# Kernel optimization log

Hardware: AMD Instinct MI355X
Metric: run time of the kernel (lower is better)

Reference implementation:

```python
import jax, jax.numpy as jnp
import numpy as np

B, T, IN_DIM, HID, OUT_DIM = 1024, 512, 64, 128, 1


def setup_inputs() -> dict:
    key = jax.random.key(0)
    ks = jax.random.split(key, 9)
    s_in = 1.0 / np.sqrt(IN_DIM)
    s_h = 1.0 / np.sqrt(HID)
    x = jax.random.normal(ks[0], (B, T, IN_DIM), dtype=jnp.float32)
    # layer 0 LSTM cell (eqx.nn.LSTMCell: weight_ih (4H,in), weight_hh (4H,H), bias (4H,))
    Wih0 = jax.random.uniform(ks[1], (4 * HID, IN_DIM), minval=-s_in, maxval=s_in, dtype=jnp.float32)
    Whh0 = jax.random.uniform(ks[2], (4 * HID, HID), minval=-s_h, maxval=s_h, dtype=jnp.float32)
    b0 = jax.random.uniform(ks[3], (4 * HID,), minval=-s_h, maxval=s_h, dtype=jnp.float32)
    # layer 1 LSTM cell
    Wih1 = jax.random.uniform(ks[4], (4 * HID, HID), minval=-s_h, maxval=s_h, dtype=jnp.float32)
    Whh1 = jax.random.uniform(ks[5], (4 * HID, HID), minval=-s_h, maxval=s_h, dtype=jnp.float32)
    b1 = jax.random.uniform(ks[6], (4 * HID,), minval=-s_h, maxval=s_h, dtype=jnp.float32)
    # output projection (eqx.nn.Linear: weight (out,in), bias (out,))
    Wout = jax.random.uniform(ks[7], (OUT_DIM, HID), minval=-s_h, maxval=s_h, dtype=jnp.float32)
    bout = jax.random.uniform(ks[8], (OUT_DIM,), minval=-s_h, maxval=s_h, dtype=jnp.float32)
    return {"x": x, "Wih0": Wih0, "Whh0": Whh0, "b0": b0,
            "Wih1": Wih1, "Whh1": Whh1, "b1": b1, "Wout": Wout, "bout": bout}


def _lstm_step(inp, h, c, Wih, Whh, b):
    # gates in i, f, g, o order (torch / equinox convention)
    z = inp @ Wih.T + h @ Whh.T + b  # (B, 4H)
    i, f, g, o = jnp.split(z, 4, axis=-1)
    c_new = jax.nn.sigmoid(f) * c + jax.nn.sigmoid(i) * jnp.tanh(g)
    h_new = jax.nn.sigmoid(o) * jnp.tanh(c_new)
    return h_new, c_new


def reference(x, Wih0, Whh0, b0, Wih1, Whh1, b1, Wout, bout):
    Bn = x.shape[0]
    xt = jnp.swapaxes(x, 0, 1)  # (T, B, in_dim): scan over time
    zeros = jnp.zeros((Bn, HID), dtype=x.dtype)
    init = (zeros, zeros, zeros, zeros)  # h0, c0, h1, c1

    def step(carry, x_t):
        h0, c0, h1, c1 = carry
        h0, c0 = _lstm_step(x_t, h0, c0, Wih0, Whh0, b0)
        h1, c1 = _lstm_step(h0, h1, c1, Wih1, Whh1, b1)
        return (h0, c0, h1, c1), None

    (h0, c0, h1, c1), _ = jax.lax.scan(step, init, xt)
    return h1 @ Wout.T + bout  # (B, out_dim)
```

## Files before the change

### kernel.cpp

```cpp
#include <hip/hip_runtime.h>
#include <math.h>

namespace {

constexpr int T_STEPS = 512;

typedef _Float16 h8v __attribute__((ext_vector_type(8)));
typedef _Float16 h2v __attribute__((ext_vector_type(2)));
typedef float    f4v __attribute__((ext_vector_type(4)));

__device__ __forceinline__ float sigf(float v) {
  return __builtin_amdgcn_rcpf(1.0f + __builtin_amdgcn_exp2f(-1.442695041f * v));
}
__device__ __forceinline__ float tanh_(float v) {
  return 2.0f * __builtin_amdgcn_rcpf(1.0f + __builtin_amdgcn_exp2f(-2.885390082f * v)) - 1.0f;
}

__global__ void pack_w(const float* __restrict__ Wih0, const float* __restrict__ Whh0,
                       const float* __restrict__ Wih1, const float* __restrict__ Whh1,
                       _Float16* __restrict__ PA, _Float16* __restrict__ PB) {
  int idx = blockIdx.x * 256 + threadIdx.x;
  if (idx < 98304) {
    int j = idx & 7, l = (idx >> 3) & 63;
    int f = idx >> 9;
    int ks = f % 6, wq = f / 6;
    int q = wq & 3, w = wq >> 2;
    int gate = 16 * (8 * q + w) + (l & 15);
    int k = 32 * ks + ((l >> 4) << 3) + j;
    float v = (k < 64) ? Wih0[gate * 64 + k] : Whh0[gate * 128 + (k - 64)];
    PA[idx] = (_Float16)v;
  } else if (idx < 98304 + 131072) {
    int i = idx - 98304;
    int j = i & 7, l = (i >> 3) & 63;
    int f = i >> 9;
    int ks = f & 7, wq = f >> 3;
    int q = wq & 3, w = wq >> 2;
    int gate = 16 * (8 * q + w) + (l & 15);
    int k = 32 * ks + ((l >> 4) << 3) + j;
    float v = (k < 128) ? Wih1[gate * 128 + k] : Whh1[gate * 128 + (k - 128)];
    PB[i] = (_Float16)v;
  }
}

__global__ __attribute__((amdgpu_waves_per_eu(2, 2))) __launch_bounds__(512)
void lstm_block(
    const float* __restrict__ x,
    const _Float16* __restrict__ PA, const _Float16* __restrict__ PB,
    const float* __restrict__ b0, const float* __restrict__ b1,
    const float* __restrict__ Wout, const float* __restrict__ bout,
    float* __restrict__ out) {
  extern __shared__ char smem[];
  h8v* whh = (h8v*)smem;
  _Float16(*h0t)[4][64][8] = (_Float16(*)[4][64][8])(smem + 131072);
  _Float16(*h1t)[4][64][8] = (_Float16(*)[4][64][8])(smem + 131072 + 8192);
  _Float16(*xt)[2][64][8]  = (_Float16(*)[2][64][8])(smem + 131072 + 16384);

  const int tid = threadIdx.x;
  const int g = blockIdx.x;
  const int w = tid >> 6, l = tid & 63;
  const int lo = l & 15, hi = l >> 4;
  const int unit = 16 * w + lo;
  const int kb_w = w >> 1;
  const int sub_w = (2 * w + (lo >> 3)) & 3;
  const int lanep = sub_w * 16 + hi * 4;
  const int jw = lo & 7;

  const h8v* PAv = (const h8v*)PA;
  const h8v* PBv = (const h8v*)PB;
  h8v W0[4][6], W1[4][4];
#pragma unroll
  for (int q = 0; q < 4; ++q) {
#pragma unroll
    for (int ks = 0; ks < 6; ++ks) W0[q][ks] = PAv[((w * 4 + q) * 6 + ks) * 64 + l];
#pragma unroll
    for (int ks = 0; ks < 4; ++ks) W1[q][ks] = PBv[((w * 4 + q) * 8 + ks) * 64 + l];
  }
#pragma unroll
  for (int q = 0; q < 4; ++q) {
#pragma unroll
    for (int ks = 0; ks < 6; ++ks) asm volatile("" : "+v"(W0[q][ks]));
#pragma unroll
    for (int ks = 0; ks < 4; ++ks) asm volatile("" : "+v"(W1[q][ks]));
  }
  float bA[4], bB[4];
#pragma unroll
  for (int q = 0; q < 4; ++q) { bA[q] = b0[unit + 128 * q]; bB[q] = b1[unit + 128 * q]; }
  float c0[4] = {0.f, 0.f, 0.f, 0.f}, c1[4] = {0.f, 0.f, 0.f, 0.f};

  for (int i = tid; i < 8192; i += 512) {
    int l2 = i & 63, f = i >> 6;
    int ks4 = f & 3, wq = f >> 2;
    whh[i] = PBv[(wq * 8 + 4 + ks4) * 64 + l2];
  }
  {
    unsigned int* z0 = (unsigned int*)h0t;
    unsigned int* z1 = (unsigned int*)h1t;
    for (int i = tid; i < 2048; i += 512) { z0[i] = 0u; z1[i] = 0u; }
    int row = tid >> 5, kk = (tid & 31) << 1;
    const float* xp = x + (((long)(g * 16 + row)) * T_STEPS + 0) * 64 + kk;
    float2 v = *(const float2*)xp;
    h2v pxv; pxv.x = (_Float16)v.x; pxv.y = (_Float16)v.y;
    *(h2v*)&xt[0][kk >> 5][(((kk >> 3) & 3) * 16) + row][kk & 7] = pxv;
  }
  __syncthreads();

  for (int j = 0; j <= T_STEPS; ++j) {
    const int p = j & 1;

    h8v h00 = *(const h8v*)&h0t[p][0][l][0];
    h8v h01 = *(const h8v*)&h0t[p][1][l][0];
    h8v h02 = *(const h8v*)&h0t[p][2][l][0];
    h8v h03 = *(const h8v*)&h0t[p][3][l][0];

    if (j < T_STEPS) {
      h8v ax0 = *(const h8v*)&xt[p][0][l][0];
      h8v ax1 = *(const h8v*)&xt[p][1][l][0];
      f4v accA[4];
#pragma unroll
      for (int q = 0; q < 4; ++q) {
        f4v z = {bA[q], bA[q], bA[q], bA[q]};
        z = __builtin_amdgcn_mfma_f32_16x16x32_f16(ax0, W0[q][0], z, 0, 0, 0);
        z = __builtin_amdgcn_mfma_f32_16x16x32_f16(ax1, W0[q][1], z, 0, 0, 0);
        z = __builtin_amdgcn_mfma_f32_16x16x32_f16(h00, W0[q][2], z, 0, 0, 0);
        z = __builtin_amdgcn_mfma_f32_16x16x32_f16(h01, W0[q][3], z, 0, 0, 0);
        z = __builtin_amdgcn_mfma_f32_16x16x32_f16(h02, W0[q][4], z, 0, 0, 0);
        z = __builtin_amdgcn_mfma_f32_16x16x32_f16(h03, W0[q][5], z, 0, 0, 0);
        accA[q] = z;
      }
#pragma unroll
      for (int r = 0; r < 4; ++r) {
        float cn = sigf(accA[1][r]) * c0[r] + sigf(accA[0][r]) * tanh_(accA[2][r]);
        c0[r] = cn;
        float hv = sigf(accA[3][r]) * tanh_(cn);
        h0t[p ^ 1][kb_w][lanep + r][jw] = (_Float16)hv;
      }
      if (j + 1 < T_STEPS) {
        int row = tid >> 5, kk = (tid & 31) << 1;
        const float* xp = x + (((long)(g * 16 + row)) * T_STEPS + (j + 1)) * 64 + kk;
        float2 v = *(const float2*)xp;
        h2v pxv; pxv.x = (_Float16)v.x; pxv.y = (_Float16)v.y;
        *(h2v*)&xt[p ^ 1][kk >> 5][(((kk >> 3) & 3) * 16) + row][kk & 7] = pxv;
      }
    }

    if (j >= 1) {
      h8v f10 = *(const h8v*)&h1t[p][0][l][0];
      h8v f11 = *(const h8v*)&h1t[p][1][l][0];
      h8v f12 = *(const h8v*)&h1t[p][2][l][0];
      h8v f13 = *(const h8v*)&h1t[p][3][l][0];
      f4v accB[4];
#pragma unroll
      for (int q = 0; q < 4; ++q) {
        const h8v* wb = &whh[((w * 4 + q) * 4) * 64 + l];
        h8v wh0 = wb[0];
        h8v wh1 = wb[64];
        h8v wh2 = wb[128];
        h8v wh3 = wb[192];
        f4v z = {bB[q], bB[q], bB[q], bB[q]};
        z = __builtin_amdgcn_mfma_f32_16x16x32_f16(h00, W1[q][0], z, 0, 0, 0);
        z = __builtin_amdgcn_mfma_f32_16x16x32_f16(h01, W1[q][1], z, 0, 0, 0);
        z = __builtin_amdgcn_mfma_f32_16x16x32_f16(h02, W1[q][2], z, 0, 0, 0);
        z = __builtin_amdgcn_mfma_f32_16x16x32_f16(h03, W1[q][3], z, 0, 0, 0);
        z = __builtin_amdgcn_mfma_f32_16x16x32_f16(f10, wh0, z, 0, 0, 0);
        z = __builtin_amdgcn_mfma_f32_16x16x32_f16(f11, wh1, z, 0, 0, 0);
        z = __builtin_amdgcn_mfma_f32_16x16x32_f16(f12, wh2, z, 0, 0, 0);
        z = __builtin_amdgcn_mfma_f32_16x16x32_f16(f13, wh3, z, 0, 0, 0);
        accB[q] = z;
      }
#pragma unroll
      for (int r = 0; r < 4; ++r) {
        float cn = sigf(accB[1][r]) * c1[r] + sigf(accB[0][r]) * tanh_(accB[2][r]);
        c1[r] = cn;
        float hv = sigf(accB[3][r]) * tanh_(cn);
        h1t[p ^ 1][kb_w][lanep + r][jw] = (_Float16)hv;
      }
    }
    __syncthreads();
  }

  if (tid < 16) {
    float acc = bout[0];
#pragma unroll 4
    for (int u = 0; u < 128; ++u) {
      float hval = (float)h1t[1][u >> 5][(((u >> 3) & 3) * 16) + tid][u & 7];
      acc = fmaf(hval, Wout[u], acc);
    }
    out[g * 16 + tid] = acc;
  }
}

}

extern "C" void kernel_launch(void* const* d_in, const int* in_sizes, int n_in,
                              void* d_out, int out_size, void* d_ws, size_t ws_size,
                              hipStream_t stream) {
  const float* x    = (const float*)d_in[0];
  const float* Wih0 = (const float*)d_in[1];
  const float* Whh0 = (const float*)d_in[2];
  const float* b0   = (const float*)d_in[3];
  const float* Wih1 = (const float*)d_in[4];
  const float* Whh1 = (const float*)d_in[5];
  const float* b1   = (const float*)d_in[6];
  const float* Wout = (const float*)d_in[7];
  const float* bout = (const float*)d_in[8];
  float* out = (float*)d_out;

  char* ws = (char*)d_ws;
  _Float16* PA = (_Float16*)ws;
  _Float16* PB = (_Float16*)(ws + 196608);

  const int lds_bytes = 131072 + 8192 + 8192 + 4096;
  hipFuncSetAttribute((const void*)lstm_block,
                      hipFuncAttributeMaxDynamicSharedMemorySize, lds_bytes);

  pack_w<<<dim3(896), dim3(256), 0, stream>>>(Wih0, Whh0, Wih1, Whh1, PA, PB);
  lstm_block<<<dim3(64), dim3(512), lds_bytes, stream>>>(
      x, PA, PB, b0, b1, Wout, bout, out);
}
```

Measured before the change: 1.291 ms.

## Split layer-0 and layer-1 LSTM work across separate wave groups

Doubles the block to 1024 threads so waves 0-7 compute layer 0 and waves 8-15 compute layer 1 at the same time, instead of each wave doing both layers in sequence. The input-to-hidden weights are no longer pinned in registers; each step reloads them from global memory (expected to hit in cache), which lowers register pressure enough for four waves per EU. The aim is to cut the serial dependent chain per timestep, at the cost of per-step global weight reloads and a larger barrier across more waves.

```diff
diff --git a/kernel.cpp b/kernel.cpp
--- a/kernel.cpp
+++ b/kernel.cpp
@@ -42,7 +42,7 @@
   }
 }
 
-__global__ __attribute__((amdgpu_waves_per_eu(2, 2))) __launch_bounds__(512)
+__global__ __attribute__((amdgpu_waves_per_eu(4, 4))) __launch_bounds__(1024)
 void lstm_block(
     const float* __restrict__ x,
     const _Float16* __restrict__ PA, const _Float16* __restrict__ PB,
@@ -57,8 +57,10 @@
 
   const int tid = threadIdx.x;
   const int g = blockIdx.x;
-  const int w = tid >> 6, l = tid & 63;
+  const int wv = tid >> 6, l = tid & 63;
   const int lo = l & 15, hi = l >> 4;
+  const bool isL0 = (wv < 8);
+  const int w = isL0 ? wv : (wv - 8);
   const int unit = 16 * w + lo;
   const int kb_w = w >> 1;
   const int sub_w = (2 * w + (lo >> 3)) & 3;
@@ -67,27 +69,14 @@
 
   const h8v* PAv = (const h8v*)PA;
   const h8v* PBv = (const h8v*)PB;
-  h8v W0[4][6], W1[4][4];
-#pragma unroll
-  for (int q = 0; q < 4; ++q) {
-#pragma unroll
-    for (int ks = 0; ks < 6; ++ks) W0[q][ks] = PAv[((w * 4 + q) * 6 + ks) * 64 + l];
-#pragma unroll
-    for (int ks = 0; ks < 4; ++ks) W1[q][ks] = PBv[((w * 4 + q) * 8 + ks) * 64 + l];
-  }
-#pragma unroll
-  for (int q = 0; q < 4; ++q) {
-#pragma unroll
-    for (int ks = 0; ks < 6; ++ks) asm volatile("" : "+v"(W0[q][ks]));
-#pragma unroll
-    for (int ks = 0; ks < 4; ++ks) asm volatile("" : "+v"(W1[q][ks]));
-  }
-  float bA[4], bB[4];
-#pragma unroll
-  for (int q = 0; q < 4; ++q) { bA[q] = b0[unit + 128 * q]; bB[q] = b1[unit + 128 * q]; }
-  float c0[4] = {0.f, 0.f, 0.f, 0.f}, c1[4] = {0.f, 0.f, 0.f, 0.f};
-
-  for (int i = tid; i < 8192; i += 512) {
+
+  float br[4];
+#pragma unroll
+  for (int q = 0; q < 4; ++q)
+    br[q] = isL0 ? b0[unit + 128 * q] : b1[unit + 128 * q];
+  float cs[4] = {0.f, 0.f, 0.f, 0.f};
+
+  for (int i = tid; i < 8192; i += 1024) {
     int l2 = i & 63, f = i >> 6;
     int ks4 = f & 3, wq = f >> 2;
     whh[i] = PBv[(wq * 8 + 4 + ks4) * 64 + l2];
@@ -95,84 +84,96 @@
   {
     unsigned int* z0 = (unsigned int*)h0t;
     unsigned int* z1 = (unsigned int*)h1t;
-    for (int i = tid; i < 2048; i += 512) { z0[i] = 0u; z1[i] = 0u; }
-    int row = tid >> 5, kk = (tid & 31) << 1;
-    const float* xp = x + (((long)(g * 16 + row)) * T_STEPS + 0) * 64 + kk;
-    float2 v = *(const float2*)xp;
-    h2v pxv; pxv.x = (_Float16)v.x; pxv.y = (_Float16)v.y;
-    *(h2v*)&xt[0][kk >> 5][(((kk >> 3) & 3) * 16) + row][kk & 7] = pxv;
+    for (int i = tid; i < 2048; i += 1024) { z0[i] = 0u; z1[i] = 0u; }
+    if (tid < 512) {
+      int row = tid >> 5, kk = (tid & 31) << 1;
+      const float* xp = x + (((long)(g * 16 + row)) * T_STEPS + 0) * 64 + kk;
+      float2 v = *(const float2*)xp;
+      h2v pxv; pxv.x = (_Float16)v.x; pxv.y = (_Float16)v.y;
+      *(h2v*)&xt[0][kk >> 5][(((kk >> 3) & 3) * 16) + row][kk & 7] = pxv;
+    }
   }
   __syncthreads();
 
   for (int j = 0; j <= T_STEPS; ++j) {
     const int p = j & 1;
 
-    h8v h00 = *(const h8v*)&h0t[p][0][l][0];
-    h8v h01 = *(const h8v*)&h0t[p][1][l][0];
-    h8v h02 = *(const h8v*)&h0t[p][2][l][0];
-    h8v h03 = *(const h8v*)&h0t[p][3][l][0];
-
-    if (j < T_STEPS) {
-      h8v ax0 = *(const h8v*)&xt[p][0][l][0];
-      h8v ax1 = *(const h8v*)&xt[p][1][l][0];
-      f4v accA[4];
-#pragma unroll
-      for (int q = 0; q < 4; ++q) {
-        f4v z = {bA[q], bA[q], bA[q], bA[q]};
-        z = __builtin_amdgcn_mfma_f32_16x16x32_f16(ax0, W0[q][0], z, 0, 0, 0);
-        z = __builtin_amdgcn_mfma_f32_16x16x32_f16(ax1, W0[q][1], z, 0, 0, 0);
-        z = __builtin_amdgcn_mfma_f32_16x16x32_f16(h00, W0[q][2], z, 0, 0, 0);
-        z = __builtin_amdgcn_mfma_f32_16x16x32_f16(h01, W0[q][3], z, 0, 0, 0);
-        z = __builtin_amdgcn_mfma_f32_16x16x32_f16(h02, W0[q][4], z, 0, 0, 0);
-        z = __builtin_amdgcn_mfma_f32_16x16x32_f16(h03, W0[q][5], z, 0, 0, 0);
-        accA[q] = z;
+    if (isL0) {
+      if (j < T_STEPS) {
+        h8v h00 = *(const h8v*)&h0t[p][0][l][0];
+        h8v h01 = *(const h8v*)&h0t[p][1][l][0];
+        h8v h02 = *(const h8v*)&h0t[p][2][l][0];
+        h8v h03 = *(const h8v*)&h0t[p][3][l][0];
+        h8v ax0 = *(const h8v*)&xt[p][0][l][0];
+        h8v ax1 = *(const h8v*)&xt[p][1][l][0];
+        f4v acc[4];
+#pragma unroll
+        for (int q = 0; q < 4; ++q) {
+          const h8v* wp = PAv + (long)((w * 4 + q) * 6) * 64 + l;
+          h8v w0 = wp[0], w1 = wp[64], w2 = wp[128];
+          h8v w3 = wp[192], w4 = wp[256], w5 = wp[320];
+          f4v z = {br[q], br[q], br[q], br[q]};
+          z = __builtin_amdgcn_mfma_f32_16x16x32_f16(ax0, w0, z, 0, 0, 0);
+          z = __builtin_amdgcn_mfma_f32_16x16x32_f16(ax1, w1, z, 0, 0, 0);
+          z = __builtin_amdgcn_mfma_f32_16x16x32_f16(h00, w2, z, 0, 0, 0);
+          z = __builtin_amdgcn_mfma_f32_16x16x32_f16(h01, w3, z, 0, 0, 0);
+          z = __builtin_amdgcn_mfma_f32_16x16x32_f16(h02, w4, z, 0, 0, 0);
+          z = __builtin_amdgcn_mfma_f32_16x16x32_f16(h03, w5, z, 0, 0, 0);
+          acc[q] = z;
+        }
+#pragma unroll
+        for (int r = 0; r < 4; ++r) {
+          float cn = sigf(acc[1][r]) * cs[r] + sigf(acc[0][r]) * tanh_(acc[2][r]);
+          cs[r] = cn;
+          float hv = sigf(acc[3][r]) * tanh_(cn);
+          h0t[p ^ 1][kb_w][lanep + r][jw] = (_Float16)hv;
+        }
+        if (j + 1 < T_STEPS) {
+          int row = tid >> 5, kk = (tid & 31) << 1;
+          const float* xp = x + (((long)(g * 16 + row)) * T_STEPS + (j + 1)) * 64 + kk;
+          float2 v = *(const float2*)xp;
+          h2v pxv; pxv.x = (_Float16)v.x; pxv.y = (_Float16)v.y;
+          *(h2v*)&xt[p ^ 1][kk >> 5][(((kk >> 3) & 3) * 16) + row][kk & 7] = pxv;
+        }
       }
-#pragma unroll
-      for (int r = 0; r < 4; ++r) {
-        float cn = sigf(accA[1][r]) * c0[r] + sigf(accA[0][r]) * tanh_(accA[2][r]);
-        c0[r] = cn;
-        float hv = sigf(accA[3][r]) * tanh_(cn);
-        h0t[p ^ 1][kb_w][lanep + r][jw] = (_Float16)hv;
-      }
-      if (j + 1 < T_STEPS) {
-        int row = tid >> 5, kk = (tid & 31) << 1;
-        const float* xp = x + (((long)(g * 16 + row)) * T_STEPS + (j + 1)) * 64 + kk;
-        float2 v = *(const float2*)xp;
-        h2v pxv; pxv.x = (_Float16)v.x; pxv.y = (_Float16)v.y;
-        *(h2v*)&xt[p ^ 1][kk >> 5][(((kk >> 3) & 3) * 16) + row][kk & 7] = pxv;
-      }
-    }
-
-    if (j >= 1) {
-      h8v f10 = *(const h8v*)&h1t[p][0][l][0];
-      h8v f11 = *(const h8v*)&h1t[p][1][l][0];
-      h8v f12 = *(const h8v*)&h1t[p][2][l][0];
-      h8v f13 = *(const h8v*)&h1t[p][3][l][0];
-      f4v accB[4];
-#pragma unroll
-      for (int q = 0; q < 4; ++q) {
-        const h8v* wb = &whh[((w * 4 + q) * 4) * 64 + l];
-        h8v wh0 = wb[0];
-        h8v wh1 = wb[64];
-        h8v wh2 = wb[128];
-        h8v wh3 = wb[192];
-        f4v z = {bB[q], bB[q], bB[q], bB[q]};
-        z = __builtin_amdgcn_mfma_f32_16x16x32_f16(h00, W1[q][0], z, 0, 0, 0);
-        z = __builtin_amdgcn_mfma_f32_16x16x32_f16(h01, W1[q][1], z, 0, 0, 0);
-        z = __builtin_amdgcn_mfma_f32_16x16x32_f16(h02, W1[q][2], z, 0, 0, 0);
-        z = __builtin_amdgcn_mfma_f32_16x16x32_f16(h03, W1[q][3], z, 0, 0, 0);
-        z = __builtin_amdgcn_mfma_f32_16x16x32_f16(f10, wh0, z, 0, 0, 0);
-        z = __builtin_amdgcn_mfma_f32_16x16x32_f16(f11, wh1, z, 0, 0, 0);
-        z = __builtin_amdgcn_mfma_f32_16x16x32_f16(f12, wh2, z, 0, 0, 0);
-        z = __builtin_amdgcn_mfma_f32_16x16x32_f16(f13, wh3, z, 0, 0, 0);
-        accB[q] = z;
-      }
-#pragma unroll
-      for (int r = 0; r < 4; ++r) {
-        float cn = sigf(accB[1][r]) * c1[r] + sigf(accB[0][r]) * tanh_(accB[2][r]);
-        c1[r] = cn;
-        float hv = sigf(accB[3][r]) * tanh_(cn);
-        h1t[p ^ 1][kb_w][lanep + r][jw] = (_Float16)hv;
+    } else {
+      if (j >= 1) {
+        h8v h00 = *(const h8v*)&h0t[p][0][l][0];
+        h8v h01 = *(const h8v*)&h0t[p][1][l][0];
+        h8v h02 = *(const h8v*)&h0t[p][2][l][0];
+        h8v h03 = *(const h8v*)&h0t[p][3][l][0];
+        h8v f10 = *(const h8v*)&h1t[p][0][l][0];
+        h8v f11 = *(const h8v*)&h1t[p][1][l][0];
+        h8v f12 = *(const h8v*)&h1t[p][2][l][0];
+        h8v f13 = *(const h8v*)&h1t[p][3][l][0];
+        f4v acc[4];
+#pragma unroll
+        for (int q = 0; q < 4; ++q) {
+          const h8v* wip = PBv + (long)((w * 4 + q) * 8) * 64 + l;
+          h8v wi0 = wip[0], wi1 = wip[64], wi2 = wip[128], wi3 = wip[192];
+          const h8v* wb = &whh[((w * 4 + q) * 4) * 64 + l];
+          h8v wh0 = wb[0];
+          h8v wh1 = wb[64];
+          h8v wh2 = wb[128];
+          h8v wh3 = wb[192];
+          f4v z = {br[q], br[q], br[q], br[q]};
+          z = __builtin_amdgcn_mfma_f32_16x16x32_f16(h00, wi0, z, 0, 0, 0);
+          z = __builtin_amdgcn_mfma_f32_16x16x32_f16(h01, wi1, z, 0, 0, 0);
+          z = __builtin_amdgcn_mfma_f32_16x16x32_f16(h02, wi2, z, 0, 0, 0);
+          z = __builtin_amdgcn_mfma_f32_16x16x32_f16(h03, wi3, z, 0, 0, 0);
+          z = __builtin_amdgcn_mfma_f32_16x16x32_f16(f10, wh0, z, 0, 0, 0);
+          z = __builtin_amdgcn_mfma_f32_16x16x32_f16(f11, wh1, z, 0, 0, 0);
+          z = __builtin_amdgcn_mfma_f32_16x16x32_f16(f12, wh2, z, 0, 0, 0);
+          z = __builtin_amdgcn_mfma_f32_16x16x32_f16(f13, wh3, z, 0, 0, 0);
+          acc[q] = z;
+        }
+#pragma unroll
+        for (int r = 0; r < 4; ++r) {
+          float cn = sigf(acc[1][r]) * cs[r] + sigf(acc[0][r]) * tanh_(acc[2][r]);
+          cs[r] = cn;
+          float hv = sigf(acc[3][r]) * tanh_(cn);
+          h1t[p ^ 1][kb_w][lanep + r][jw] = (_Float16)hv;
+        }
       }
     }
     __syncthreads();
@@ -214,6 +215,6 @@
                       hipFuncAttributeMaxDynamicSharedMemorySize, lds_bytes);
 
   pack_w<<<dim3(896), dim3(256), 0, stream>>>(Wih0, Whh0, Wih1, Whh1, PA, PB);
-  lstm_block<<<dim3(64), dim3(512), lds_bytes, stream>>>(
+  lstm_block<<<dim3(64), dim3(1024), lds_bytes, stream>>>(
       x, PA, PB, b0, b1, Wout, bout, out);
 }
```

After: 1.797 ms. 1.39x slower.
